# Kernel tuning notes

Hardware: AMD Instinct MI355X
Metric: run time of the kernel (lower is better)

## Reference

```python
import jax, jax.numpy as jnp
import numpy as np

IN_DIM, HIDDEN_DIM, OUT_DIM = 128, 64, 64
N_NODES, N_EDGES = 100000, 1000000


def gcn_layer(x, src, dst, W, b):
    """PyG GCNConv: h = W x; out = D^-1/2 (A+I) D^-1/2 h + b (self-loops already in src/dst)."""
    n = x.shape[0]
    deg = jax.ops.segment_sum(jnp.ones_like(src, dtype=x.dtype), dst, num_segments=n)
    dinv = jnp.where(deg > 0, jax.lax.rsqrt(deg), 0.0)
    norm = dinv[src] * dinv[dst]          # [E+N]
    h = x @ W                              # [N, out]
    msg = h[src] * norm[:, None]           # [E+N, out] gather + scale
    out = jax.ops.segment_sum(msg, dst, num_segments=n)  # scatter-add
    return out + b


def setup_inputs() -> dict:
    key = jax.random.key(0)
    k1, k2, k3, k4 = jax.random.split(key, 4)
    x = jax.random.normal(k1, (N_NODES, IN_DIM), dtype=jnp.float32)
    edge_index = jax.random.randint(k2, (2, N_EDGES), 0, N_NODES, dtype=jnp.int64)
    # Glorot-ish init for the two GCNConv linear weights; zero biases (PyG default)
    W1 = jax.random.normal(k3, (IN_DIM, HIDDEN_DIM), dtype=jnp.float32) / np.sqrt(IN_DIM)
    W2 = jax.random.normal(k4, (HIDDEN_DIM, OUT_DIM), dtype=jnp.float32) / np.sqrt(HIDDEN_DIM)
    b1 = jnp.zeros((HIDDEN_DIM,), dtype=jnp.float32)
    b2 = jnp.zeros((OUT_DIM,), dtype=jnp.float32)
    return {"x": x, "edge_index": edge_index, "W1": W1, "b1": b1, "W2": W2, "b2": b2}


def reference(x, edge_index, W1, b1, W2, b2):
    n = x.shape[0]
    loops = jnp.arange(n, dtype=edge_index.dtype)
    src = jnp.concatenate([edge_index[0], loops])  # add self-loops once
    dst = jnp.concatenate([edge_index[1], loops])
    x1 = gcn_layer(x, src, dst, W1, b1)
    h = jax.nn.relu(x1)
    # dropout is identity in eval/reference mode
    x2 = gcn_layer(h, src, dst, W2, b2)
    return x2
```

## Files before the change

### kernel.cpp

```cpp
#include <hip/hip_runtime.h>
#include <hip/hip_fp16.h>

#define DIM_IN 128
#define DIM_HID 64
#define BK_SHIFT 9
#define BK_SIZE 512
#define SRC_BITS 17
#define CAP 6144

typedef _Float16 half8 __attribute__((ext_vector_type(8)));
typedef _Float16 half4v __attribute__((ext_vector_type(4)));
typedef float floatx4 __attribute__((ext_vector_type(4)));


#define P_EPT  16
#define P_TILE 4096

__global__ __launch_bounds__(256)
void partition_kernel(const int* __restrict__ src, const int* __restrict__ dst,
                      int* __restrict__ bcur, int* __restrict__ part, int E) {
    __shared__ int hist[256];
    __shared__ int bofs[256];
    __shared__ int gbase[256];
    __shared__ int stage[P_TILE];
    __shared__ unsigned char auxb[P_TILE];
    const int tid   = threadIdx.x;
    const int tile0 = blockIdx.x * P_TILE;
    const int tcnt  = min(P_TILE, E - tile0);

    hist[tid] = 0;
    __syncthreads();

    int pack[P_EPT], bb[P_EPT], lo[P_EPT];
#pragma unroll
    for (int i = 0; i < P_EPT; ++i) {
        int e = tile0 + i * 256 + tid;
        bb[i] = -1;
        if (e < E) {
            int d = dst[e];
            int s = src[e];
            bb[i]   = d >> BK_SHIFT;
            pack[i] = ((d & (BK_SIZE - 1)) << SRC_BITS) | s;
            lo[i]   = atomicAdd(&hist[bb[i]], 1);
        }
    }
    __syncthreads();

    bofs[tid] = hist[tid];
    __syncthreads();
    for (int off = 1; off < 256; off <<= 1) {
        int t = (tid >= off) ? bofs[tid - off] : 0;
        __syncthreads();
        bofs[tid] += t;
        __syncthreads();
    }
    int ex = bofs[tid] - hist[tid];
    __syncthreads();
    bofs[tid] = ex;
    if (hist[tid]) gbase[tid] = tid * CAP + atomicAdd(&bcur[tid], hist[tid]);
    __syncthreads();

#pragma unroll
    for (int i = 0; i < P_EPT; ++i) {
        if (bb[i] >= 0) {
            int p = bofs[bb[i]] + lo[i];
            stage[p] = pack[i];
            auxb[p]  = (unsigned char)bb[i];
        }
    }
    __syncthreads();

    for (int k = tid; k < tcnt; k += 256) {
        int b = auxb[k];
        part[gbase[b] + (k - bofs[b])] = stage[k];
    }
}


__global__ __launch_bounds__(256)
void bucket_fill_kernel(const int* __restrict__ bcur, const int* __restrict__ part,
                        int2* __restrict__ nodeinfo, float* __restrict__ dinv,
                        int* __restrict__ srcs, int n) {
    __shared__ int cnt[BK_SIZE];
    __shared__ int rp[BK_SIZE];
    __shared__ int s2[256];
    const int tid   = threadIdx.x;
    const int bid   = blockIdx.x;
    const int node0 = bid << BK_SHIFT;
    const int bs    = min(BK_SIZE, n - node0);
    const int ebase = bid * CAP;
    const int ecnt  = bcur[bid];

    cnt[tid] = 0; cnt[tid + 256] = 0;
    __syncthreads();
    for (int k = tid; k < ecnt; k += 256)
        atomicAdd(&cnt[part[ebase + k] >> SRC_BITS], 1);
    __syncthreads();

    int a  = cnt[2 * tid];
    int b2 = cnt[2 * tid + 1];
    s2[tid] = a + b2;
    __syncthreads();
    for (int off = 1; off < 256; off <<= 1) {
        int t = (tid >= off) ? s2[tid - off] : 0;
        __syncthreads();
        s2[tid] += t;
        __syncthreads();
    }
    int ex = s2[tid] - (a + b2);
    rp[2 * tid]     = ex;
    rp[2 * tid + 1] = ex + a;
    __syncthreads();

    for (int i = tid; i < bs; i += 256) {
        nodeinfo[node0 + i] = make_int2(ebase + rp[i], cnt[i]);
        dinv[node0 + i]     = rsqrtf((float)cnt[i] + 1.0f);
    }
    __syncthreads();

    cnt[tid] = 0; cnt[tid + 256] = 0;
    __syncthreads();
    for (int k = tid; k < ecnt; k += 256) {
        int v    = part[ebase + k];
        int li   = v >> SRC_BITS;
        int slot = atomicAdd(&cnt[li], 1);
        srcs[ebase + rp[li] + slot] = v & ((1 << SRC_BITS) - 1);
    }
}


template <int K, bool RELU>
__launch_bounds__(256)
__global__ void gemm_mfma_kernel(const float* __restrict__ x, const float* __restrict__ W,
                                 const float* __restrict__ dinv, _Float16* __restrict__ out,
                                 int n) {
    constexpr int LDK = K + 8;
    __shared__ _Float16 Wt[64 * LDK];
    const int tid = threadIdx.x;

    for (int idx = tid; idx < K * 64; idx += 256) {
        int k = idx >> 6, c = idx & 63;
        Wt[c * LDK + k] = (_Float16)W[idx];
    }
    __syncthreads();

    const int wave = tid >> 6;
    const int lane = tid & 63;
    const int r    = lane & 15;
    const int g    = lane >> 4;
    const int row0 = blockIdx.x * 64 + wave * 16;
    const int arow = row0 + r;
    const float* xrow = x + (size_t)(arow < n ? arow : 0) * K + g * 8;

    floatx4 acc0 = {}, acc1 = {}, acc2 = {}, acc3 = {};

#pragma unroll
    for (int kt = 0; kt < K / 32; ++kt) {
        float4 a0 = *(const float4*)(xrow + kt * 32);
        float4 a1 = *(const float4*)(xrow + kt * 32 + 4);
        if (RELU) {
            a0.x = fmaxf(a0.x, 0.f); a0.y = fmaxf(a0.y, 0.f);
            a0.z = fmaxf(a0.z, 0.f); a0.w = fmaxf(a0.w, 0.f);
            a1.x = fmaxf(a1.x, 0.f); a1.y = fmaxf(a1.y, 0.f);
            a1.z = fmaxf(a1.z, 0.f); a1.w = fmaxf(a1.w, 0.f);
        }
        half8 a;
        a[0] = (_Float16)a0.x; a[1] = (_Float16)a0.y;
        a[2] = (_Float16)a0.z; a[3] = (_Float16)a0.w;
        a[4] = (_Float16)a1.x; a[5] = (_Float16)a1.y;
        a[6] = (_Float16)a1.z; a[7] = (_Float16)a1.w;

        const _Float16* wb = &Wt[r * LDK + kt * 32 + g * 8];
        half8 b0 = *(const half8*)(wb + 0 * 16 * LDK);
        half8 b1 = *(const half8*)(wb + 1 * 16 * LDK);
        half8 b2 = *(const half8*)(wb + 2 * 16 * LDK);
        half8 b3 = *(const half8*)(wb + 3 * 16 * LDK);
        acc0 = __builtin_amdgcn_mfma_f32_16x16x32_f16(a, b0, acc0, 0, 0, 0);
        acc1 = __builtin_amdgcn_mfma_f32_16x16x32_f16(a, b1, acc1, 0, 0, 0);
        acc2 = __builtin_amdgcn_mfma_f32_16x16x32_f16(a, b2, acc2, 0, 0, 0);
        acc3 = __builtin_amdgcn_mfma_f32_16x16x32_f16(a, b3, acc3, 0, 0, 0);
    }

#pragma unroll
    for (int j = 0; j < 4; ++j) {
        int drow = row0 + g * 4 + j;
        if (drow < n) {
            float dn = dinv[drow];
            _Float16* o = out + (size_t)drow * 64 + r;
            o[0]  = (_Float16)(acc0[j] * dn);
            o[16] = (_Float16)(acc1[j] * dn);
            o[32] = (_Float16)(acc2[j] * dn);
            o[48] = (_Float16)(acc3[j] * dn);
        }
    }
}


__global__ __launch_bounds__(256)
void gather_kernel(const int2* __restrict__ nodeinfo, const int* __restrict__ srcs,
                   const float* __restrict__ dinv, const half4v* __restrict__ hs,
                   const float4* __restrict__ b, float4* __restrict__ out, int n) {
    const int tid  = threadIdx.x;
    const int f    = tid & 15;
    const int node = blockIdx.x * 16 + (tid >> 4);
    if (node >= n) return;

    int2 info = nodeinfo[node];
    int start = info.x, c = info.y;

    half4v v = hs[(size_t)node * 16 + f];
    float4 acc = make_float4((float)v[0], (float)v[1], (float)v[2], (float)v[3]);

    int j = 0;
    for (; j + 4 <= c; j += 4) {
        int s0 = srcs[start + j + 0];
        int s1 = srcs[start + j + 1];
        int s2 = srcs[start + j + 2];
        int s3 = srcs[start + j + 3];
        half4v v0 = hs[(size_t)s0 * 16 + f];
        half4v v1 = hs[(size_t)s1 * 16 + f];
        half4v v2 = hs[(size_t)s2 * 16 + f];
        half4v v3 = hs[(size_t)s3 * 16 + f];
        acc.x += (float)v0[0] + (float)v1[0] + (float)v2[0] + (float)v3[0];
        acc.y += (float)v0[1] + (float)v1[1] + (float)v2[1] + (float)v3[1];
        acc.z += (float)v0[2] + (float)v1[2] + (float)v2[2] + (float)v3[2];
        acc.w += (float)v0[3] + (float)v1[3] + (float)v2[3] + (float)v3[3];
    }
    for (; j < c; ++j) {
        int s = srcs[start + j];
        half4v vv = hs[(size_t)s * 16 + f];
        acc.x += (float)vv[0]; acc.y += (float)vv[1];
        acc.z += (float)vv[2]; acc.w += (float)vv[3];
    }

    float dn = dinv[node];
    float4 bb = b[f];
    out[(size_t)node * 16 + f] = make_float4(fmaf(acc.x, dn, bb.x), fmaf(acc.y, dn, bb.y),
                                             fmaf(acc.z, dn, bb.z), fmaf(acc.w, dn, bb.w));
}


extern "C" void kernel_launch(void* const* d_in, const int* in_sizes, int n_in,
                              void* d_out, int out_size, void* d_ws, size_t ws_size,
                              hipStream_t stream) {
    const float* x   = (const float*)d_in[0];
    const int*   ei  = (const int*)d_in[1];
    const float* W1  = (const float*)d_in[2];
    const float* b1  = (const float*)d_in[3];
    const float* W2  = (const float*)d_in[4];
    const float* b2  = (const float*)d_in[5];
    float*       out = (float*)d_out;

    const int n = in_sizes[0] / DIM_IN;
    const int E = in_sizes[1] / 2;
    const int* srcp = ei;
    const int* dstp = ei + E;
    const int NB = (n + BK_SIZE - 1) >> BK_SHIFT;

    const int npad = ((n + 255) / 256) * 256;

    int*      bcur     = (int*)d_ws;
    int2*     nodeinfo = (int2*)(bcur + 256);
    float*    dinv     = (float*)((int*)nodeinfo + 2 * npad);
    int*      srcs     = (int*)(dinv + npad);
    float*    agg      = (float*)(srcs + (size_t)NB * CAP);
    _Float16* h        = (_Float16*)(agg + (size_t)n * 64);
    int*      part     = (int*)agg;

    const int gb = (n + 63) / 64;
    const int ab = (n + 15) / 16;
    const int pb = (E + P_TILE - 1) / P_TILE;

    hipMemsetAsync(bcur, 0, 256 * 4, stream);

    partition_kernel<<<pb, 256, 0, stream>>>(srcp, dstp, bcur, part, E);
    bucket_fill_kernel<<<NB, 256, 0, stream>>>(bcur, part, nodeinfo, dinv, srcs, n);

    gemm_mfma_kernel<DIM_IN, false><<<gb, 256, 0, stream>>>(x, W1, dinv, h, n);
    gather_kernel<<<ab, 256, 0, stream>>>(nodeinfo, srcs, dinv, (const half4v*)h,
                                          (const float4*)b1, (float4*)agg, n);

    gemm_mfma_kernel<DIM_HID, true><<<gb, 256, 0, stream>>>(agg, W2, dinv, h, n);
    gather_kernel<<<ab, 256, 0, stream>>>(nodeinfo, srcs, dinv, (const half4v*)h,
                                          (const float4*)b2, (float4*)out, n);
}
```

Baseline: 120.6 us.

## Pad CSR rows with zero-row sentinels, store layer-1 output in fp16, widen gather

The per-node neighbor lists are padded to multiples of four using a sentinel index that points at a zeroed padding row of h. This removes the remainder loop in the gather. The intermediate layer-1 aggregate is now stored as fp16 instead of fp32, and the second GEMM reads it directly, which halves that traffic. The gather now uses 8 lanes per node with 16-byte half8 loads instead of 16 lanes with 8-byte loads. The memset is replaced by a tiny zero kernel. The padding adds extra gather loads for the sentinel rows, and fp16 storage of the hidden activations reduces precision.

```diff
diff --git a/kernel.cpp b/kernel.cpp
--- a/kernel.cpp
+++ b/kernel.cpp
@@ -7,10 +7,13 @@
 #define BK_SIZE 512
 #define SRC_BITS 17
 #define CAP 6144
+#define CAP2 8192
 
 typedef _Float16 half8 __attribute__((ext_vector_type(8)));
-typedef _Float16 half4v __attribute__((ext_vector_type(4)));
 typedef float floatx4 __attribute__((ext_vector_type(4)));
+
+
+__global__ void zero_kernel(int* __restrict__ p) { p[threadIdx.x] = 0; }
 
 
 #define P_EPT  16
@@ -80,26 +83,28 @@
 __global__ __launch_bounds__(256)
 void bucket_fill_kernel(const int* __restrict__ bcur, const int* __restrict__ part,
                         int2* __restrict__ nodeinfo, float* __restrict__ dinv,
-                        int* __restrict__ srcs, int n) {
+                        int* __restrict__ srcs, int n, int zrow) {
     __shared__ int cnt[BK_SIZE];
     __shared__ int rp[BK_SIZE];
     __shared__ int s2[256];
+    __shared__ int total;
     const int tid   = threadIdx.x;
     const int bid   = blockIdx.x;
     const int node0 = bid << BK_SHIFT;
     const int bs    = min(BK_SIZE, n - node0);
-    const int ebase = bid * CAP;
+    const int pbase = bid * CAP;
+    const int sbase = bid * CAP2;
     const int ecnt  = bcur[bid];
 
     cnt[tid] = 0; cnt[tid + 256] = 0;
     __syncthreads();
     for (int k = tid; k < ecnt; k += 256)
-        atomicAdd(&cnt[part[ebase + k] >> SRC_BITS], 1);
-    __syncthreads();
-
-    int a  = cnt[2 * tid];
-    int b2 = cnt[2 * tid + 1];
-    s2[tid] = a + b2;
+        atomicAdd(&cnt[part[pbase + k] >> SRC_BITS], 1);
+    __syncthreads();
+
+    int c0 = cnt[2 * tid], c1 = cnt[2 * tid + 1];
+    int p0 = (c0 + 3) & ~3, p1 = (c1 + 3) & ~3;
+    s2[tid] = p0 + p1;
     __syncthreads();
     for (int off = 1; off < 256; off <<= 1) {
         int t = (tid >= off) ? s2[tid - off] : 0;
@@ -107,31 +112,34 @@
         s2[tid] += t;
         __syncthreads();
     }
-    int ex = s2[tid] - (a + b2);
+    int ex = s2[tid] - (p0 + p1);
     rp[2 * tid]     = ex;
-    rp[2 * tid + 1] = ex + a;
+    rp[2 * tid + 1] = ex + p0;
+    if (tid == 255) total = s2[255];
     __syncthreads();
 
     for (int i = tid; i < bs; i += 256) {
-        nodeinfo[node0 + i] = make_int2(ebase + rp[i], cnt[i]);
-        dinv[node0 + i]     = rsqrtf((float)cnt[i] + 1.0f);
+        int c = cnt[i];
+        nodeinfo[node0 + i] = make_int2(sbase + rp[i], (c + 3) & ~3);
+        dinv[node0 + i]     = rsqrtf((float)c + 1.0f);
     }
     __syncthreads();
 
     cnt[tid] = 0; cnt[tid + 256] = 0;
+    for (int k = tid; k < total; k += 256) srcs[sbase + k] = zrow;
     __syncthreads();
     for (int k = tid; k < ecnt; k += 256) {
-        int v    = part[ebase + k];
+        int v    = part[pbase + k];
         int li   = v >> SRC_BITS;
         int slot = atomicAdd(&cnt[li], 1);
-        srcs[ebase + rp[li] + slot] = v & ((1 << SRC_BITS) - 1);
-    }
-}
-
-
-template <int K, bool RELU>
+        srcs[sbase + rp[li] + slot] = v & ((1 << SRC_BITS) - 1);
+    }
+}
+
+
+template <int K, bool RELU, typename T>
 __launch_bounds__(256)
-__global__ void gemm_mfma_kernel(const float* __restrict__ x, const float* __restrict__ W,
+__global__ void gemm_mfma_kernel(const T* __restrict__ x, const float* __restrict__ W,
                                  const float* __restrict__ dinv, _Float16* __restrict__ out,
                                  int n) {
     constexpr int LDK = K + 8;
@@ -150,25 +158,34 @@
     const int g    = lane >> 4;
     const int row0 = blockIdx.x * 64 + wave * 16;
     const int arow = row0 + r;
-    const float* xrow = x + (size_t)(arow < n ? arow : 0) * K + g * 8;
+    const T* xrow = x + (size_t)(arow < n ? arow : 0) * K + g * 8;
 
     floatx4 acc0 = {}, acc1 = {}, acc2 = {}, acc3 = {};
 
 #pragma unroll
     for (int kt = 0; kt < K / 32; ++kt) {
-        float4 a0 = *(const float4*)(xrow + kt * 32);
-        float4 a1 = *(const float4*)(xrow + kt * 32 + 4);
-        if (RELU) {
-            a0.x = fmaxf(a0.x, 0.f); a0.y = fmaxf(a0.y, 0.f);
-            a0.z = fmaxf(a0.z, 0.f); a0.w = fmaxf(a0.w, 0.f);
-            a1.x = fmaxf(a1.x, 0.f); a1.y = fmaxf(a1.y, 0.f);
-            a1.z = fmaxf(a1.z, 0.f); a1.w = fmaxf(a1.w, 0.f);
+        half8 a;
+        if constexpr (sizeof(T) == 4) {
+            float4 a0 = *(const float4*)(xrow + kt * 32);
+            float4 a1 = *(const float4*)(xrow + kt * 32 + 4);
+            if (RELU) {
+                a0.x = fmaxf(a0.x, 0.f); a0.y = fmaxf(a0.y, 0.f);
+                a0.z = fmaxf(a0.z, 0.f); a0.w = fmaxf(a0.w, 0.f);
+                a1.x = fmaxf(a1.x, 0.f); a1.y = fmaxf(a1.y, 0.f);
+                a1.z = fmaxf(a1.z, 0.f); a1.w = fmaxf(a1.w, 0.f);
+            }
+            a[0] = (_Float16)a0.x; a[1] = (_Float16)a0.y;
+            a[2] = (_Float16)a0.z; a[3] = (_Float16)a0.w;
+            a[4] = (_Float16)a1.x; a[5] = (_Float16)a1.y;
+            a[6] = (_Float16)a1.z; a[7] = (_Float16)a1.w;
+        } else {
+            a = *(const half8*)(xrow + kt * 32);
+            if (RELU) {
+#pragma unroll
+                for (int i = 0; i < 8; ++i)
+                    a[i] = a[i] > (_Float16)0 ? a[i] : (_Float16)0;
+            }
         }
-        half8 a;
-        a[0] = (_Float16)a0.x; a[1] = (_Float16)a0.y;
-        a[2] = (_Float16)a0.z; a[3] = (_Float16)a0.w;
-        a[4] = (_Float16)a1.x; a[5] = (_Float16)a1.y;
-        a[6] = (_Float16)a1.z; a[7] = (_Float16)a1.w;
 
         const _Float16* wb = &Wt[r * LDK + kt * 32 + g * 8];
         half8 b0 = *(const half8*)(wb + 0 * 16 * LDK);
@@ -184,59 +201,70 @@
 #pragma unroll
     for (int j = 0; j < 4; ++j) {
         int drow = row0 + g * 4 + j;
+        _Float16* o = out + (size_t)drow * 64 + r;
         if (drow < n) {
             float dn = dinv[drow];
-            _Float16* o = out + (size_t)drow * 64 + r;
             o[0]  = (_Float16)(acc0[j] * dn);
             o[16] = (_Float16)(acc1[j] * dn);
             o[32] = (_Float16)(acc2[j] * dn);
             o[48] = (_Float16)(acc3[j] * dn);
+        } else {
+            o[0] = (_Float16)0; o[16] = (_Float16)0;
+            o[32] = (_Float16)0; o[48] = (_Float16)0;
         }
     }
 }
 
 
+template <typename OUT>
 __global__ __launch_bounds__(256)
 void gather_kernel(const int2* __restrict__ nodeinfo, const int* __restrict__ srcs,
-                   const float* __restrict__ dinv, const half4v* __restrict__ hs,
-                   const float4* __restrict__ b, float4* __restrict__ out, int n) {
+                   const float* __restrict__ dinv, const half8* __restrict__ hs,
+                   const float* __restrict__ b, OUT* __restrict__ out, int n) {
     const int tid  = threadIdx.x;
-    const int f    = tid & 15;
-    const int node = blockIdx.x * 16 + (tid >> 4);
+    const int f    = tid & 7;
+    const int node = blockIdx.x * 32 + (tid >> 3);
     if (node >= n) return;
 
     int2 info = nodeinfo[node];
-    int start = info.x, c = info.y;
-
-    half4v v = hs[(size_t)node * 16 + f];
-    float4 acc = make_float4((float)v[0], (float)v[1], (float)v[2], (float)v[3]);
-
-    int j = 0;
-    for (; j + 4 <= c; j += 4) {
+    int start = info.x, cpad = info.y;
+
+    half8 sv = hs[(size_t)node * 8 + f];
+    float acc[8];
+#pragma unroll
+    for (int i = 0; i < 8; ++i) acc[i] = (float)sv[i];
+
+    for (int j = 0; j < cpad; j += 4) {
         int s0 = srcs[start + j + 0];
         int s1 = srcs[start + j + 1];
         int s2 = srcs[start + j + 2];
         int s3 = srcs[start + j + 3];
-        half4v v0 = hs[(size_t)s0 * 16 + f];
-        half4v v1 = hs[(size_t)s1 * 16 + f];
-        half4v v2 = hs[(size_t)s2 * 16 + f];
-        half4v v3 = hs[(size_t)s3 * 16 + f];
-        acc.x += (float)v0[0] + (float)v1[0] + (float)v2[0] + (float)v3[0];
-        acc.y += (float)v0[1] + (float)v1[1] + (float)v2[1] + (float)v3[1];
-        acc.z += (float)v0[2] + (float)v1[2] + (float)v2[2] + (float)v3[2];
-        acc.w += (float)v0[3] + (float)v1[3] + (float)v2[3] + (float)v3[3];
-    }
-    for (; j < c; ++j) {
-        int s = srcs[start + j];
-        half4v vv = hs[(size_t)s * 16 + f];
-        acc.x += (float)vv[0]; acc.y += (float)vv[1];
-        acc.z += (float)vv[2]; acc.w += (float)vv[3];
+        half8 v0 = hs[(size_t)s0 * 8 + f];
+        half8 v1 = hs[(size_t)s1 * 8 + f];
+        half8 v2 = hs[(size_t)s2 * 8 + f];
+        half8 v3 = hs[(size_t)s3 * 8 + f];
+#pragma unroll
+        for (int i = 0; i < 8; ++i)
+            acc[i] += ((float)v0[i] + (float)v1[i]) + ((float)v2[i] + (float)v3[i]);
     }
 
     float dn = dinv[node];
-    float4 bb = b[f];
-    out[(size_t)node * 16 + f] = make_float4(fmaf(acc.x, dn, bb.x), fmaf(acc.y, dn, bb.y),
-                                             fmaf(acc.z, dn, bb.z), fmaf(acc.w, dn, bb.w));
+    if constexpr (sizeof(OUT) == 2) {
+        half8 o;
+#pragma unroll
+        for (int i = 0; i < 8; ++i) o[i] = (_Float16)fmaf(acc[i], dn, b[f * 8 + i]);
+        ((half8*)out)[(size_t)node * 8 + f] = o;
+    } else {
+        const float4* b4 = (const float4*)b;
+        float4 bb0 = b4[f * 2], bb1 = b4[f * 2 + 1];
+        float4 o0 = make_float4(fmaf(acc[0], dn, bb0.x), fmaf(acc[1], dn, bb0.y),
+                                fmaf(acc[2], dn, bb0.z), fmaf(acc[3], dn, bb0.w));
+        float4 o1 = make_float4(fmaf(acc[4], dn, bb1.x), fmaf(acc[5], dn, bb1.y),
+                                fmaf(acc[6], dn, bb1.z), fmaf(acc[7], dn, bb1.w));
+        float4* o4 = (float4*)out;
+        o4[(size_t)node * 16 + f * 2]     = o0;
+        o4[(size_t)node * 16 + f * 2 + 1] = o1;
+    }
 }
 
 
@@ -255,7 +283,8 @@
     const int E = in_sizes[1] / 2;
     const int* srcp = ei;
     const int* dstp = ei + E;
-    const int NB = (n + BK_SIZE - 1) >> BK_SHIFT;
+    const int NB    = (n + BK_SIZE - 1) >> BK_SHIFT;
+    const int nrows = ((n + 63) / 64) * 64;
 
     const int npad = ((n + 255) / 256) * 256;
 
@@ -263,24 +292,23 @@
     int2*     nodeinfo = (int2*)(bcur + 256);
     float*    dinv     = (float*)((int*)nodeinfo + 2 * npad);
     int*      srcs     = (int*)(dinv + npad);
-    float*    agg      = (float*)(srcs + (size_t)NB * CAP);
-    _Float16* h        = (_Float16*)(agg + (size_t)n * 64);
-    int*      part     = (int*)agg;
+    _Float16* g1       = (_Float16*)(srcs + (size_t)NB * CAP2);
+    _Float16* h        = g1 + (size_t)n * 64;
+    int*      part     = (int*)g1;
 
     const int gb = (n + 63) / 64;
-    const int ab = (n + 15) / 16;
+    const int ab = (n + 31) / 32;
     const int pb = (E + P_TILE - 1) / P_TILE;
 
-    hipMemsetAsync(bcur, 0, 256 * 4, stream);
-
+    zero_kernel<<<1, 256, 0, stream>>>(bcur);
     partition_kernel<<<pb, 256, 0, stream>>>(srcp, dstp, bcur, part, E);
-    bucket_fill_kernel<<<NB, 256, 0, stream>>>(bcur, part, nodeinfo, dinv, srcs, n);
-
-    gemm_mfma_kernel<DIM_IN, false><<<gb, 256, 0, stream>>>(x, W1, dinv, h, n);
-    gather_kernel<<<ab, 256, 0, stream>>>(nodeinfo, srcs, dinv, (const half4v*)h,
-                                          (const float4*)b1, (float4*)agg, n);
-
-    gemm_mfma_kernel<DIM_HID, true><<<gb, 256, 0, stream>>>(agg, W2, dinv, h, n);
-    gather_kernel<<<ab, 256, 0, stream>>>(nodeinfo, srcs, dinv, (const half4v*)h,
-                                          (const float4*)b2, (float4*)out, n);
-}
+    bucket_fill_kernel<<<NB, 256, 0, stream>>>(bcur, part, nodeinfo, dinv, srcs, n, n);
+
+    gemm_mfma_kernel<DIM_IN, false, float><<<gb, 256, 0, stream>>>(x, W1, dinv, h, n);
+    gather_kernel<_Float16><<<ab, 256, 0, stream>>>(nodeinfo, srcs, dinv, (const half8*)h,
+                                                    b1, g1, n);
+
+    gemm_mfma_kernel<DIM_HID, true, _Float16><<<gb, 256, 0, stream>>>(g1, W2, dinv, h, n);
+    gather_kernel<float><<<ab, 256, 0, stream>>>(nodeinfo, srcs, dinv, (const half8*)h,
+                                                 b2, out, n);
+}
```

New measurement: 111.5 us. 7.5% less time.
